# Optimization experiments

Hardware: AMD Instinct MI355X
Metric: run time of the kernel (lower is better)

Reference implementation:

```python
import jax, jax.numpy as jnp
import numpy as np

# Dims matching init_kwargs / input_specs
H = 8          # num_heads
S = 256        # seq_len_src
T = 1024       # seq_len_tgt
D = 64         # head_dim
SZ_B = 16      # batch size
B = SZ_B * H   # flattened batch*heads = 128
RATIO = T // S # subsampling_ratio = 4
NEG = -100.0   # pad value used by the skewing trick


def setup_inputs() -> dict:
    key = jax.random.key(0)
    kq, k1, k2 = jax.random.split(key, 3)
    q = jax.random.normal(kq, (B, T, D), dtype=jnp.float32)
    e1 = jax.random.normal(k1, (H * S, D), dtype=jnp.float32)
    e2 = jax.random.normal(k2, (H * S, D), dtype=jnp.float32)
    return {"q": q, "e1": e1, "e2": e2}


def _rel_scores(q, e):
    # torch: e.repeat(sz_b,1,1).view(sz_b*H, S, D); einsum('bld,bmd->blm', q, e)
    # equivalent: per-head einsum without materializing the tiled e
    qh = q.reshape(SZ_B, H, T, D)
    eh = e.reshape(H, S, D)
    return jnp.einsum('bhtd,hsd->bhts', qh, eh).reshape(B, T, S)


def _skew(r, prepend_pad):
    # Music-Transformer skewing: (B,T,S) -> reinterpret as (B,S,T), pad a
    # -100 column (front for e1 path, back for e2 path), pad -100 rows to
    # (B,T,T+1), then reshape by S to shift scores into relative positions.
    r = r.reshape(B, S, T)
    pad_col = jnp.full((B, S, 1), NEG, dtype=r.dtype)
    parts = [pad_col, r] if prepend_pad else [r, pad_col]
    r = jnp.concatenate(parts, axis=2)                       # (B, S, T+1)
    if T > S:
        pad_rows = jnp.full((B, T - S, T + 1), NEG, dtype=r.dtype)
        r = jnp.concatenate([r, pad_rows], axis=1)           # (B, T, T+1)
    r = r.reshape(B, -1, S)                                  # (B, T*(T+1)//S, S)
    if prepend_pad:
        r = r[:, 1:]
    return r[:, :T]                                          # (B, T, S)


def reference(q, e1, e2):
    r1 = _skew(_rel_scores(q, e1), prepend_pad=True)
    r2 = _skew(_rel_scores(q, e2), prepend_pad=False)
    # masks_up: triu(k=1); masks_down: triu(k=0).flip(0).flip(1) == tril(k=0)
    # both repeat_interleave'd by RATIO along the row (tgt) axis -> (T, S)
    up = jnp.repeat(jnp.triu(jnp.ones((S, S), dtype=bool), 1), RATIO, axis=0)
    down = jnp.repeat(jnp.tril(jnp.ones((S, S), dtype=bool), 0), RATIO, axis=0)
    r1 = jnp.where(up[None, :, :], jnp.array(0.0, r1.dtype), r1)
    r2 = jnp.where(down[None, :, :], jnp.array(0.0, r2.dtype), r2)
    return r1 + r2
```

## Files before the change

kernel.cpp:

```cpp
#include <hip/hip_runtime.h>

#define NH   8
#define NS   256
#define NT   1024
#define ND   64

typedef __attribute__((ext_vector_type(4))) float f32x4;
typedef __attribute__((ext_vector_type(8))) short short8;

__device__ __forceinline__ short f2bf(float f) {
    union { float f; unsigned u; } v; v.f = f;
    unsigned r = v.u + 0x7FFFu + ((v.u >> 16) & 1u);
    return (short)(r >> 16);
}

__global__ __launch_bounds__(256, 4) void srel_kernel(
    const float* __restrict__ q, const float* __restrict__ e1,
    const float* __restrict__ e2, float* __restrict__ out)
{
    const int h   = blockIdx.x >> 8;
    const int a   = blockIdx.x & 255;
    const int tid = threadIdx.x;
    const int wave = tid >> 6;
    const int lane = tid & 63;

    __shared__ __align__(16) char smem[64*64*2 + NS*64*2];
    unsigned short* lA = (unsigned short*)smem;
    unsigned short* lB = (unsigned short*)(smem + 64*64*2);
    float* fbuf = (float*)smem;

    {
        const int rr = tid >> 3;
        const int pc = tid & 7;
        #pragma unroll
        for (int g = 0; g < 8; ++g) {
            const int s  = g * 32 + rr;
            const int lc = pc ^ (s & 7);
            const float* srcrow = (s <= a)
                ? (e1 + ((size_t)(h * NS + 255 - a + s)) * ND)
                : (e2 + ((size_t)(h * NS + s - a)) * ND);
            const f32x4* src = (const f32x4*)(srcrow + lc * 8);
            f32x4 v0 = src[0];
            f32x4 v1 = src[1];
            short8 pk;
            pk[0]=f2bf(v0[0]); pk[1]=f2bf(v0[1]); pk[2]=f2bf(v0[2]); pk[3]=f2bf(v0[3]);
            pk[4]=f2bf(v1[0]); pk[5]=f2bf(v1[1]); pk[6]=f2bf(v1[2]); pk[7]=f2bf(v1[3]);
            *(short8*)(lB + s * 64 + pc * 8) = pk;
        }
    }

    {
        const int m    = tid >> 2;
        const int part = tid & 3;
        const int b    = (m >> 2) * NH + h;
        const int t    = a * 4 + (m & 3);
        const f32x4* src = (const f32x4*)(q + ((size_t)b * NT + t) * ND + part * 16);
        f32x4 v0 = __builtin_nontemporal_load(src + 0);
        f32x4 v1 = __builtin_nontemporal_load(src + 1);
        f32x4 v2 = __builtin_nontemporal_load(src + 2);
        f32x4 v3 = __builtin_nontemporal_load(src + 3);
        short8 p0, p1;
        p0[0]=f2bf(v0[0]); p0[1]=f2bf(v0[1]); p0[2]=f2bf(v0[2]); p0[3]=f2bf(v0[3]);
        p0[4]=f2bf(v1[0]); p0[5]=f2bf(v1[1]); p0[6]=f2bf(v1[2]); p0[7]=f2bf(v1[3]);
        p1[0]=f2bf(v2[0]); p1[1]=f2bf(v2[1]); p1[2]=f2bf(v2[2]); p1[3]=f2bf(v2[3]);
        p1[4]=f2bf(v3[0]); p1[5]=f2bf(v3[1]); p1[6]=f2bf(v3[2]); p1[7]=f2bf(v3[3]);
        const int sw = m & 7;
        *(short8*)(lA + m * 64 + (((2*part)   ^ sw) * 8)) = p0;
        *(short8*)(lA + m * 64 + (((2*part+1) ^ sw) * 8)) = p1;
    }

    __syncthreads();

    const int lrow = lane & 15;
    const int quad = lane >> 4;
    f32x4 acc[4][4] = {};
    #pragma unroll
    for (int kk2 = 0; kk2 < 2; ++kk2) {
        const int swz = ((4 * kk2 + quad) ^ (lrow & 7)) * 8;
        short8 afr[4], bfr[4];
        #pragma unroll
        for (int tm = 0; tm < 4; ++tm)
            afr[tm] = *(const short8*)(lA + (tm * 16 + lrow) * 64 + swz);
        #pragma unroll
        for (int tn = 0; tn < 4; ++tn)
            bfr[tn] = *(const short8*)(lB + (wave * 64 + tn * 16 + lrow) * 64 + swz);
        #pragma unroll
        for (int tm = 0; tm < 4; ++tm)
            #pragma unroll
            for (int tn = 0; tn < 4; ++tn)
                acc[tm][tn] = __builtin_amdgcn_mfma_f32_16x16x32_bf16(
                    afr[tm], bfr[tn], acc[tm][tn], 0, 0, 0);
    }

    #pragma unroll
    for (int c = 0; c < 2; ++c) {
        __syncthreads();
        #pragma unroll
        for (int tmh = 0; tmh < 2; ++tmh) {
            const int tm = c * 2 + tmh;
            #pragma unroll
            for (int r = 0; r < 4; ++r) {
                const int rl = tmh * 16 + quad * 4 + r;
                #pragma unroll
                for (int tn = 0; tn < 4; ++tn)
                    fbuf[rl * 260 + wave * 64 + tn * 16 + lrow] = acc[tm][tn][r];
            }
        }
        __syncthreads();
        #pragma unroll
        for (int i = 0; i < 8; ++i) {
            const int rl = i * 4 + wave;
            const int m  = c * 32 + rl;
            const int b  = (m >> 2) * NH + h;
            const int t  = a * 4 + (m & 3);
            f32x4 v = *(const f32x4*)(fbuf + rl * 260 + lane * 4);
            __builtin_nontemporal_store(v, (f32x4*)(out + ((size_t)b * NT + t) * NS + lane * 4));
        }
    }
}

extern "C" void kernel_launch(void* const* d_in, const int* in_sizes, int n_in,
                              void* d_out, int out_size, void* d_ws, size_t ws_size,
                              hipStream_t stream) {
    (void)in_sizes; (void)n_in; (void)ws_size; (void)out_size; (void)d_ws;
    const float* q  = (const float*)d_in[0];
    const float* e1 = (const float*)d_in[1];
    const float* e2 = (const float*)d_in[2];
    float* out = (float*)d_out;

    srel_kernel<<<dim3(NH * NS), dim3(256), 0, stream>>>(q, e1, e2, out);
}
```

Measured before the change: 177.3 us.

## Load relative embeddings straight into MFMA B fragments, skipping LDS staging

The B operand (the skewed e1/e2 rows) is now read from global memory directly into registers in MFMA fragment layout and converted to bf16 there, instead of being staged through LDS. This drops the LDS B buffer, shrinking shared memory from 40KB to about 33KB, which may allow more blocks per CU, and removes one store/load round trip. Nontemporal loads of q and nontemporal stores of the output are replaced with ordinary accesses. The tradeoff is less coalesced global reads of the e rows, since each lane fetches 32-byte pieces of separate rows, with the memory latency now sitting inside the MFMA loop.

Result: faster. 170.3 us (-4.0%).

```diff
diff --git a/kernel.cpp b/kernel.cpp
--- a/kernel.cpp
+++ b/kernel.cpp
@@ -24,30 +24,9 @@
     const int wave = tid >> 6;
     const int lane = tid & 63;
 
-    __shared__ __align__(16) char smem[64*64*2 + NS*64*2];
+    __shared__ __align__(16) char smem[33280];
     unsigned short* lA = (unsigned short*)smem;
-    unsigned short* lB = (unsigned short*)(smem + 64*64*2);
     float* fbuf = (float*)smem;
-
-    {
-        const int rr = tid >> 3;
-        const int pc = tid & 7;
-        #pragma unroll
-        for (int g = 0; g < 8; ++g) {
-            const int s  = g * 32 + rr;
-            const int lc = pc ^ (s & 7);
-            const float* srcrow = (s <= a)
-                ? (e1 + ((size_t)(h * NS + 255 - a + s)) * ND)
-                : (e2 + ((size_t)(h * NS + s - a)) * ND);
-            const f32x4* src = (const f32x4*)(srcrow + lc * 8);
-            f32x4 v0 = src[0];
-            f32x4 v1 = src[1];
-            short8 pk;
-            pk[0]=f2bf(v0[0]); pk[1]=f2bf(v0[1]); pk[2]=f2bf(v0[2]); pk[3]=f2bf(v0[3]);
-            pk[4]=f2bf(v1[0]); pk[5]=f2bf(v1[1]); pk[6]=f2bf(v1[2]); pk[7]=f2bf(v1[3]);
-            *(short8*)(lB + s * 64 + pc * 8) = pk;
-        }
-    }
 
     {
         const int m    = tid >> 2;
@@ -55,10 +34,7 @@
         const int b    = (m >> 2) * NH + h;
         const int t    = a * 4 + (m & 3);
         const f32x4* src = (const f32x4*)(q + ((size_t)b * NT + t) * ND + part * 16);
-        f32x4 v0 = __builtin_nontemporal_load(src + 0);
-        f32x4 v1 = __builtin_nontemporal_load(src + 1);
-        f32x4 v2 = __builtin_nontemporal_load(src + 2);
-        f32x4 v3 = __builtin_nontemporal_load(src + 3);
+        f32x4 v0 = src[0], v1 = src[1], v2 = src[2], v3 = src[3];
         short8 p0, p1;
         p0[0]=f2bf(v0[0]); p0[1]=f2bf(v0[1]); p0[2]=f2bf(v0[2]); p0[3]=f2bf(v0[3]);
         p0[4]=f2bf(v1[0]); p0[5]=f2bf(v1[1]); p0[6]=f2bf(v1[2]); p0[7]=f2bf(v1[3]);
@@ -69,21 +45,37 @@
         *(short8*)(lA + m * 64 + (((2*part+1) ^ sw) * 8)) = p1;
     }
 
+    const int lrow = lane & 15;
+    const int quad = lane >> 4;
+    const float* rp[4];
+    #pragma unroll
+    for (int tn = 0; tn < 4; ++tn) {
+        const int s = wave * 64 + tn * 16 + lrow;
+        rp[tn] = (s <= a)
+            ? (e1 + ((size_t)(h * NS + 255 - a + s)) * ND)
+            : (e2 + ((size_t)(h * NS + s - a)) * ND);
+    }
+
     __syncthreads();
 
-    const int lrow = lane & 15;
-    const int quad = lane >> 4;
     f32x4 acc[4][4] = {};
     #pragma unroll
     for (int kk2 = 0; kk2 < 2; ++kk2) {
-        const int swz = ((4 * kk2 + quad) ^ (lrow & 7)) * 8;
+        const int lc  = 4 * kk2 + quad;
+        const int swz = (lc ^ (lrow & 7)) * 8;
         short8 afr[4], bfr[4];
+        #pragma unroll
+        for (int tn = 0; tn < 4; ++tn) {
+            const f32x4* bp = (const f32x4*)(rp[tn] + lc * 8);
+            f32x4 v0 = bp[0], v1 = bp[1];
+            short8 pk;
+            pk[0]=f2bf(v0[0]); pk[1]=f2bf(v0[1]); pk[2]=f2bf(v0[2]); pk[3]=f2bf(v0[3]);
+            pk[4]=f2bf(v1[0]); pk[5]=f2bf(v1[1]); pk[6]=f2bf(v1[2]); pk[7]=f2bf(v1[3]);
+            bfr[tn] = pk;
+        }
         #pragma unroll
         for (int tm = 0; tm < 4; ++tm)
             afr[tm] = *(const short8*)(lA + (tm * 16 + lrow) * 64 + swz);
-        #pragma unroll
-        for (int tn = 0; tn < 4; ++tn)
-            bfr[tn] = *(const short8*)(lB + (wave * 64 + tn * 16 + lrow) * 64 + swz);
         #pragma unroll
         for (int tm = 0; tm < 4; ++tm)
             #pragma unroll
@@ -114,7 +106,7 @@
             const int b  = (m >> 2) * NH + h;
             const int t  = a * 4 + (m & 3);
             f32x4 v = *(const f32x4*)(fbuf + rl * 260 + lane * 4);
-            __builtin_nontemporal_store(v, (f32x4*)(out + ((size_t)b * NT + t) * NS + lane * 4));
+            *(f32x4*)(out + ((size_t)b * NT + t) * NS + lane * 4) = v;
         }
     }
 }
```
